# Optimization experiments

Measured on AMD Instinct MI355X. Metric: run time of the kernel, lower is better.

Reference implementation:

```python
import jax, jax.numpy as jnp
import numpy as np

LEN = 2048

def setup_inputs() -> dict:
    key = jax.random.key(0)
    k1, k2 = jax.random.split(key)
    x = jax.random.normal(k1, (LEN,), dtype=jnp.float32)
    y = jax.random.normal(k2, (LEN,), dtype=jnp.float32)
    return {"x": x, "y": y}

def reference(x, y):
    # Classic DTW DP with squared-difference cost.
    # Original torch code clamps indices with max(i-1,0)/max(j-1,0); because
    # DTW[i,j] is still +inf when read, the clamped reads reduce to the
    # standard recurrence: row 0 is a cumulative sum, col 0 uses only 'up',
    # interior uses min(up, left, diag).
    inf = jnp.float32(jnp.inf)
    cost0 = (x[0] - y) ** 2            # [len2]
    row0 = jnp.cumsum(cost0)           # DTW row i=0

    def row_step(prev_row, xi):
        cost = (xi - y) ** 2                                   # [len2]
        diag = jnp.concatenate([prev_row[:1], prev_row[:-1]])  # prev_row[j-1], clamped at j=0
        def cell(left, cud):
            c, up, dg = cud
            v = c + jnp.minimum(jnp.minimum(up, left), dg)
            return v, v
        # left init = inf => at j=0 min reduces to min(up, diag) = prev_row[0]
        _, new_row = jax.lax.scan(cell, inf, (cost, prev_row, diag))
        return new_row, None

    last_row, _ = jax.lax.scan(row_step, row0, x[1:])
    return jnp.sqrt(last_row[-1])
```

## Files before the change

### kernel.cpp

```cpp
#include <hip/hip_runtime.h>
#include <math.h>


#define NLEN   2048
#define NWL    4
#define CSTEP  64
#define SPB    (CSTEP / 2)
#define DSKEW  192
#define EXTRA  64
#define PAD    128
#define RROW   (PAD + 2176)
#define YPAD   128
#define TAUMAX 2112
#define GTOT   (TAUMAX + 7 * DSKEW + EXTRA + CSTEP)
#define FLAGBIG (1 << 20)
#define INFV   1e30f

typedef float f32x2 __attribute__((ext_vector_type(2)));

__device__ __forceinline__ float dpp_shr1(float v, float inj) {
    int r = __builtin_amdgcn_update_dpp(
        __builtin_bit_cast(int, inj), __builtin_bit_cast(int, v),
        0x138 , 0xF, 0xF, false );
    return __builtin_bit_cast(float, r);
}
__device__ __forceinline__ float rdlane(float v, int l) {
    return __builtin_bit_cast(float,
        __builtin_amdgcn_readlane(__builtin_bit_cast(int, v), l));
}
__device__ __forceinline__ float min3f(float a, float b, float c) {
    unsigned ia = __builtin_bit_cast(unsigned, a);
    unsigned ib = __builtin_bit_cast(unsigned, b);
    unsigned ic = __builtin_bit_cast(unsigned, c);
    unsigned m  = __builtin_elementwise_min(
                      __builtin_elementwise_min(ia, ib), ic);
    return __builtin_bit_cast(float, m);
}
__device__ __forceinline__ void spinflag(int* flag, int target) {
    while (__hip_atomic_load(flag, __ATOMIC_ACQUIRE,
                             __HIP_MEMORY_SCOPE_AGENT) < target)
        __builtin_amdgcn_s_sleep(2);
}

__global__ __launch_bounds__(256, 1) void dtw_kernel(const float* __restrict__ X,
                                                     const float* __restrict__ Y,
                                                     float* __restrict__ out,
                                                     float* __restrict__ ws) {
    int*   flag = (int*)ws;
    float* grow = ws + 16 + PAD;

    __shared__ __align__(16) float yB[YPAD + NLEN + YPAD];
    __shared__ float ring[(NWL + 1) * RROW];
    float* yS = yB + YPAD;

    const int tid  = threadIdx.x;
    const int w    = tid >> 6;
    const int lane = tid & 63;
    const int b    = blockIdx.x;
    const int skew = (4 * b + w) * DSKEW + (b ? EXTRA : 0);
    const bool isprod = (b == 0) & (w == 3);
    const bool iscons = (b == 1) & (w == 0);

    {
        const float4* Y4 = (const float4*)Y;
        float4* y4 = (float4*)(yB + YPAD);
        y4[tid]       = Y4[tid];
        y4[tid + 256] = Y4[tid + 256];
        if (tid < YPAD) {
            yB[tid]               = INFV;
            yB[YPAD + NLEN + tid] = INFV;
        }
    }
    for (int k = tid; k < (NWL + 1) * RROW; k += 256) ring[k] = INFV;
    __syncthreads();

    f32x2 xx0, xx1, xx2, xx3;
    {
        const float4 xa = *(const float4*)&X[b * 1024 + w * 256 + lane * 4];
        xx0 = (f32x2){xa.x, xa.x}; xx1 = (f32x2){xa.y, xa.y};
        xx2 = (f32x2){xa.z, xa.z}; xx3 = (f32x2){xa.w, xa.w};
    }

    float pB0 = INFV, pB1 = INFV, pB2 = INFV, pB3 = INFV;
    float a3p = INFV;
    float uBp = (b == 0 && tid == 0) ? 0.0f : INFV;
    float gcur = INFV, gnext = INFV;

    const float* ringR = ring + w * RROW + PAD;
    float*       ringW = ring + (w + 1) * RROW + PAD;

    for (int gb = 0; gb < GTOT; gb += CSTEP) {
        const int tau0 = gb - skew;

        if (tau0 >= 0 && tau0 <= TAUMAX) {
            float rblk;
            if (iscons) {
                if (tau0 == 0) {
                    spinflag(flag, 63);
                    gcur = grow[lane];
                }
                const int nt = tau0 + CSTEP;
                if (nt <= TAUMAX) {
                    int tgt = nt + 63;
                    if (tgt > NLEN - 1) tgt = NLEN - 1;
                    spinflag(flag, tgt);
                    gnext = grow[nt + lane];
                }
                rblk = gcur;
            } else {
                rblk = ringR[tau0 + lane];
            }

            f32x2 y2[SPB];
            {
                const f32x2* yp = (const f32x2*)(yS + (tau0 - 2 * lane));
                #pragma unroll
                for (int k = 0; k < SPB; ++k) y2[k] = yp[k];
            }
            float* wp = ringW + (tau0 - 2 * lane);
            const bool isout = (b == 1) & (w == 3) & (lane == 63)
                             & (tau0 == TAUMAX);

            #pragma unroll
            for (int s = 0; s < SPB; ++s) {
                const float riA = rdlane(rblk, 2 * s);
                const float riB = rdlane(rblk, 2 * s + 1);
                const float uA  = dpp_shr1(a3p, riA);
                const float uB  = dpp_shr1(pB3, riB);
                const f32x2 yv = y2[s];
                f32x2 d0 = xx0 - yv;
                float n0A = fmaf(d0.x, d0.x, min3f(pB0, uA,  uBp));
                float n0B = fmaf(d0.y, d0.y, min3f(n0A, uB,  uA));
                f32x2 d1 = xx1 - yv;
                float n1A = fmaf(d1.x, d1.x, min3f(pB1, n0A, pB0));
                float n1B = fmaf(d1.y, d1.y, min3f(n1A, n0B, n0A));
                f32x2 d2 = xx2 - yv;
                float n2A = fmaf(d2.x, d2.x, min3f(pB2, n1A, pB1));
                float n2B = fmaf(d2.y, d2.y, min3f(n2A, n1B, n1A));
                f32x2 d3 = xx3 - yv;
                float n3A = fmaf(d3.x, d3.x, min3f(pB3, n2A, pB2));
                float n3B = fmaf(d3.y, d3.y, min3f(n3A, n2B, n2A));
                f32x2 wv; wv.x = n3A; wv.y = n3B;
                *(f32x2*)(wp + 2 * s) = wv;
                uBp = uB; a3p = n3A;
                pB0 = n0B; pB1 = n1B; pB2 = n2B; pB3 = n3B;
                if (s == 30 && isout) out[0] = sqrtf(n3B);
            }

            if (isprod) {
                if (tau0 >= 128) {
                    __threadfence();
                    if (lane == 0)
                        __hip_atomic_store(flag, tau0 - 127, __ATOMIC_RELEASE,
                                           __HIP_MEMORY_SCOPE_AGENT);
                }
                grow[tau0 - 126 + lane] = ringW[tau0 - 126 + lane];
                if (tau0 == TAUMAX) {
                    __threadfence();
                    if (lane == 0)
                        __hip_atomic_store(flag, FLAGBIG, __ATOMIC_RELEASE,
                                           __HIP_MEMORY_SCOPE_AGENT);
                }
            }
            if (iscons) gcur = gnext;
        }
        __syncthreads();
    }
}

#define FNW    4
#define FGTOT  (TAUMAX + (FNW - 1) * DSKEW + CSTEP)

__global__ __launch_bounds__(256, 1) void dtw_kernel_fb(const float* __restrict__ X,
                                                        const float* __restrict__ Y,
                                                        float* __restrict__ out) {
    __shared__ __align__(16) float yB[YPAD + NLEN + YPAD];
    __shared__ float ring[(FNW + 1) * RROW];
    float* yS = yB + YPAD;

    const int tid  = threadIdx.x;
    const int w    = tid >> 6;
    const int lane = tid & 63;

    {
        const float4* Y4 = (const float4*)Y;
        float4* y4 = (float4*)(yB + YPAD);
        y4[tid]       = Y4[tid];
        y4[tid + 256] = Y4[tid + 256];
        if (tid < YPAD) {
            yB[tid]               = INFV;
            yB[YPAD + NLEN + tid] = INFV;
        }
    }
    for (int k = tid; k < (FNW + 1) * RROW; k += 256) ring[k] = INFV;
    __syncthreads();

    f32x2 xx0, xx1, xx2, xx3, xx4, xx5, xx6, xx7;
    {
        const float4 xa = *(const float4*)&X[tid * 8];
        const float4 xb = *(const float4*)&X[tid * 8 + 4];
        xx0 = (f32x2){xa.x, xa.x}; xx1 = (f32x2){xa.y, xa.y};
        xx2 = (f32x2){xa.z, xa.z}; xx3 = (f32x2){xa.w, xa.w};
        xx4 = (f32x2){xb.x, xb.x}; xx5 = (f32x2){xb.y, xb.y};
        xx6 = (f32x2){xb.z, xb.z}; xx7 = (f32x2){xb.w, xb.w};
    }

    float pB0 = INFV, pB1 = INFV, pB2 = INFV, pB3 = INFV;
    float pB4 = INFV, pB5 = INFV, pB6 = INFV, pB7 = INFV;
    float a7p = INFV;
    float uBp = (tid == 0) ? 0.0f : INFV;

    const float* ringR = ring + w * RROW + PAD;
    float*       ringW = ring + (w + 1) * RROW + PAD;

    for (int gb = 0; gb < FGTOT; gb += CSTEP) {
        const int tau0 = gb - w * DSKEW;

        if (tau0 >= 0 && tau0 <= TAUMAX) {
            const float rblk = ringR[tau0 + lane];
            f32x2 y2[SPB];
            {
                const f32x2* yp = (const f32x2*)(yS + (tau0 - 2 * lane));
                #pragma unroll
                for (int k = 0; k < SPB; ++k) y2[k] = yp[k];
            }
            float* wp = ringW + (tau0 - 2 * lane);
            const bool isout = (tau0 == TAUMAX) & (w == FNW - 1) & (lane == 63);

            #pragma unroll
            for (int s = 0; s < SPB; ++s) {
                const float riA = rdlane(rblk, 2 * s);
                const float riB = rdlane(rblk, 2 * s + 1);
                const float uA  = dpp_shr1(a7p, riA);
                const float uB  = dpp_shr1(pB7, riB);
                const f32x2 yv = y2[s];
                f32x2 d0 = xx0 - yv;
                float n0A = fmaf(d0.x, d0.x, min3f(pB0, uA,  uBp));
                float n0B = fmaf(d0.y, d0.y, min3f(n0A, uB,  uA));
                f32x2 d1 = xx1 - yv;
                float n1A = fmaf(d1.x, d1.x, min3f(pB1, n0A, pB0));
                float n1B = fmaf(d1.y, d1.y, min3f(n1A, n0B, n0A));
                f32x2 d2 = xx2 - yv;
                float n2A = fmaf(d2.x, d2.x, min3f(pB2, n1A, pB1));
                float n2B = fmaf(d2.y, d2.y, min3f(n2A, n1B, n1A));
                f32x2 d3 = xx3 - yv;
                float n3A = fmaf(d3.x, d3.x, min3f(pB3, n2A, pB2));
                float n3B = fmaf(d3.y, d3.y, min3f(n3A, n2B, n2A));
                f32x2 d4 = xx4 - yv;
                float n4A = fmaf(d4.x, d4.x, min3f(pB4, n3A, pB3));
                float n4B = fmaf(d4.y, d4.y, min3f(n4A, n3B, n3A));
                f32x2 d5 = xx5 - yv;
                float n5A = fmaf(d5.x, d5.x, min3f(pB5, n4A, pB4));
                float n5B = fmaf(d5.y, d5.y, min3f(n5A, n4B, n4A));
                f32x2 d6 = xx6 - yv;
                float n6A = fmaf(d6.x, d6.x, min3f(pB6, n5A, pB5));
                float n6B = fmaf(d6.y, d6.y, min3f(n6A, n5B, n5A));
                f32x2 d7 = xx7 - yv;
                float n7A = fmaf(d7.x, d7.x, min3f(pB7, n6A, pB6));
                float n7B = fmaf(d7.y, d7.y, min3f(n7A, n6B, n6A));
                f32x2 wv; wv.x = n7A; wv.y = n7B;
                *(f32x2*)(wp + 2 * s) = wv;
                uBp = uB; a7p = n7A;
                pB0 = n0B; pB1 = n1B; pB2 = n2B; pB3 = n3B;
                pB4 = n4B; pB5 = n5B; pB6 = n6B; pB7 = n7B;
                if (s == 30 && isout) out[0] = sqrtf(n7B);
            }
        }
        __syncthreads();
    }
}

extern "C" void kernel_launch(void* const* d_in, const int* in_sizes, int n_in,
                              void* d_out, int out_size, void* d_ws, size_t ws_size,
                              hipStream_t stream) {
    const float* x = (const float*)d_in[0];
    const float* y = (const float*)d_in[1];
    (void)in_sizes; (void)n_in; (void)out_size;
    if (d_ws != nullptr && ws_size >= 16384) {
        hipMemsetAsync(d_ws, 0, 4, stream);
        dtw_kernel<<<2, 256, 0, stream>>>(x, y, (float*)d_out, (float*)d_ws);
    } else {
        dtw_kernel_fb<<<1, 256, 0, stream>>>(x, y, (float*)d_out);
    }
}
```

Before: 180.6 us.

## Split DTW wavefront across four blocks with two rows per lane and ring buffers

Spreads the anti-diagonal DTW pipeline across four workgroups instead of two, so each lane owns two rows of x instead of four and the column step halves to 32. Inter-block boundary rows go through per-block global ring buffers with their own flags, and the consumer prefetches the next chunk into shared scratch. Boundary values are now read from LDS as vectors instead of via per-step readlane. The aim is a shorter serial dependency chain per step, paid for with more pipeline fill and drain stages and more cross-block flag spinning on the critical path.

```diff
diff --git a/kernel.cpp b/kernel.cpp
--- a/kernel.cpp
+++ b/kernel.cpp
@@ -4,29 +4,27 @@
 
 #define NLEN   2048
 #define NWL    4
-#define CSTEP  64
+#define CSTEP  32
 #define SPB    (CSTEP / 2)
-#define DSKEW  192
+#define DSKEW  160
 #define EXTRA  64
 #define PAD    128
-#define RROW   (PAD + 2176)
+#define RROW   2304
 #define YPAD   128
-#define TAUMAX 2112
-#define GTOT   (TAUMAX + 7 * DSKEW + EXTRA + CSTEP)
+#define TAUMAX 2144
+#define GTOT   (TAUMAX + 15 * DSKEW + 3 * EXTRA + CSTEP)
+#define RMASK  1023
 #define FLAGBIG (1 << 20)
 #define INFV   1e30f
 
 typedef float f32x2 __attribute__((ext_vector_type(2)));
+typedef float f32x4 __attribute__((ext_vector_type(4)));
 
 __device__ __forceinline__ float dpp_shr1(float v, float inj) {
     int r = __builtin_amdgcn_update_dpp(
         __builtin_bit_cast(int, inj), __builtin_bit_cast(int, v),
         0x138 , 0xF, 0xF, false );
     return __builtin_bit_cast(float, r);
-}
-__device__ __forceinline__ float rdlane(float v, int l) {
-    return __builtin_bit_cast(float,
-        __builtin_amdgcn_readlane(__builtin_bit_cast(int, v), l));
 }
 __device__ __forceinline__ float min3f(float a, float b, float c) {
     unsigned ia = __builtin_bit_cast(unsigned, a);
@@ -41,25 +39,34 @@
                              __HIP_MEMORY_SCOPE_AGENT) < target)
         __builtin_amdgcn_s_sleep(2);
 }
+__device__ __forceinline__ float gload(const float* p) {
+    unsigned u = __hip_atomic_load((const unsigned*)p, __ATOMIC_RELAXED,
+                                   __HIP_MEMORY_SCOPE_AGENT);
+    return __builtin_bit_cast(float, u);
+}
 
 __global__ __launch_bounds__(256, 1) void dtw_kernel(const float* __restrict__ X,
                                                      const float* __restrict__ Y,
                                                      float* __restrict__ out,
                                                      float* __restrict__ ws) {
-    int*   flag = (int*)ws;
-    float* grow = ws + 16 + PAD;
-
     __shared__ __align__(16) float yB[YPAD + NLEN + YPAD];
-    __shared__ float ring[(NWL + 1) * RROW];
+    __shared__ __align__(16) float ring[(NWL + 1) * RROW];
+    __shared__ __align__(16) float cscr[32];
     float* yS = yB + YPAD;
 
     const int tid  = threadIdx.x;
     const int w    = tid >> 6;
     const int lane = tid & 63;
     const int b    = blockIdx.x;
-    const int skew = (4 * b + w) * DSKEW + (b ? EXTRA : 0);
-    const bool isprod = (b == 0) & (w == 3);
-    const bool iscons = (b == 1) & (w == 0);
+    const int skew = (4 * b + w) * DSKEW + b * EXTRA;
+    const bool isprod = (b < 3) & (w == 3);
+    const bool iscons = (b > 0) & (w == 0);
+    const bool isbot  = (b == 3) & (w == 3);
+
+    int*   flagp = (int*)ws + 64 * b;
+    int*   flagc = (int*)ws + 64 * (b - 1);
+    float* growp = (float*)ws + 256 + 1024 * b;
+    float* growc = (float*)ws + 256 + 1024 * (b - 1);
 
     {
         const float4* Y4 = (const float4*)Y;
@@ -74,17 +81,16 @@
     for (int k = tid; k < (NWL + 1) * RROW; k += 256) ring[k] = INFV;
     __syncthreads();
 
-    f32x2 xx0, xx1, xx2, xx3;
+    f32x2 xx0, xx1;
     {
-        const float4 xa = *(const float4*)&X[b * 1024 + w * 256 + lane * 4];
-        xx0 = (f32x2){xa.x, xa.x}; xx1 = (f32x2){xa.y, xa.y};
-        xx2 = (f32x2){xa.z, xa.z}; xx3 = (f32x2){xa.w, xa.w};
-    }
-
-    float pB0 = INFV, pB1 = INFV, pB2 = INFV, pB3 = INFV;
-    float a3p = INFV;
+        const float2 xa = *(const float2*)&X[b * 512 + w * 128 + lane * 2];
+        xx0 = (f32x2){xa.x, xa.x};
+        xx1 = (f32x2){xa.y, xa.y};
+    }
+
+    float pB0 = INFV, pB1 = INFV;
+    float a1p = INFV;
     float uBp = (b == 0 && tid == 0) ? 0.0f : INFV;
-    float gcur = INFV, gnext = INFV;
 
     const float* ringR = ring + w * RROW + PAD;
     float*       ringW = ring + (w + 1) * RROW + PAD;
@@ -93,23 +99,34 @@
         const int tau0 = gb - skew;
 
         if (tau0 >= 0 && tau0 <= TAUMAX) {
-            float rblk;
+            if (isprod && tau0 >= 128) {
+                __threadfence();
+                if (lane == 0)
+                    __hip_atomic_store(flagp, tau0 - 127, __ATOMIC_RELEASE,
+                                       __HIP_MEMORY_SCOPE_AGENT);
+            }
+
+            float pref = 0.0f;
+            const bool dopref = iscons & (tau0 + CSTEP <= TAUMAX);
             if (iscons) {
                 if (tau0 == 0) {
-                    spinflag(flag, 63);
-                    gcur = grow[lane];
-                }
-                const int nt = tau0 + CSTEP;
-                if (nt <= TAUMAX) {
-                    int tgt = nt + 63;
-                    if (tgt > NLEN - 1) tgt = NLEN - 1;
-                    spinflag(flag, tgt);
-                    gnext = grow[nt + lane];
-                }
-                rblk = gcur;
-            } else {
-                rblk = ringR[tau0 + lane];
-            }
+                    spinflag(flagc, 31);
+                    if (lane < 32)
+                        cscr[lane] = gload(growc + ((lane + 2048) & RMASK));
+                }
+                if (dopref) {
+                    const int nt = tau0 + CSTEP;
+                    int tgt = nt + 31; if (tgt > NLEN - 1) tgt = NLEN - 1;
+                    spinflag(flagc, tgt);
+                    if (lane < 32)
+                        pref = gload(growc + ((nt + lane + 2048) & RMASK));
+                }
+            }
+
+            const float* rsrc = iscons ? cscr : (ringR + tau0);
+            f32x4 rv[8];
+            #pragma unroll
+            for (int q = 0; q < 8; ++q) rv[q] = *(const f32x4*)(rsrc + 4 * q);
 
             f32x2 y2[SPB];
             {
@@ -118,15 +135,14 @@
                 for (int k = 0; k < SPB; ++k) y2[k] = yp[k];
             }
             float* wp = ringW + (tau0 - 2 * lane);
-            const bool isout = (b == 1) & (w == 3) & (lane == 63)
-                             & (tau0 == TAUMAX);
+            const bool isout = isbot & (lane == 63) & (tau0 == TAUMAX);
 
             #pragma unroll
             for (int s = 0; s < SPB; ++s) {
-                const float riA = rdlane(rblk, 2 * s);
-                const float riB = rdlane(rblk, 2 * s + 1);
-                const float uA  = dpp_shr1(a3p, riA);
-                const float uB  = dpp_shr1(pB3, riB);
+                const float riA = rv[(2 * s) >> 2][(2 * s) & 3];
+                const float riB = rv[(2 * s + 1) >> 2][(2 * s + 1) & 3];
+                const float uA  = dpp_shr1(a1p, riA);
+                const float uB  = dpp_shr1(pB1, riB);
                 const f32x2 yv = y2[s];
                 f32x2 d0 = xx0 - yv;
                 float n0A = fmaf(d0.x, d0.x, min3f(pB0, uA,  uBp));
@@ -134,48 +150,52 @@
                 f32x2 d1 = xx1 - yv;
                 float n1A = fmaf(d1.x, d1.x, min3f(pB1, n0A, pB0));
                 float n1B = fmaf(d1.y, d1.y, min3f(n1A, n0B, n0A));
-                f32x2 d2 = xx2 - yv;
-                float n2A = fmaf(d2.x, d2.x, min3f(pB2, n1A, pB1));
-                float n2B = fmaf(d2.y, d2.y, min3f(n2A, n1B, n1A));
-                f32x2 d3 = xx3 - yv;
-                float n3A = fmaf(d3.x, d3.x, min3f(pB3, n2A, pB2));
-                float n3B = fmaf(d3.y, d3.y, min3f(n3A, n2B, n2A));
-                f32x2 wv; wv.x = n3A; wv.y = n3B;
-                *(f32x2*)(wp + 2 * s) = wv;
-                uBp = uB; a3p = n3A;
-                pB0 = n0B; pB1 = n1B; pB2 = n2B; pB3 = n3B;
-                if (s == 30 && isout) out[0] = sqrtf(n3B);
+                if (!isbot) {
+                    f32x2 wv; wv.x = n1A; wv.y = n1B;
+                    *(f32x2*)(wp + 2 * s) = wv;
+                }
+                uBp = uB; a1p = n1A;
+                pB0 = n0B; pB1 = n1B;
+                if (s == 14 && isout) out[0] = sqrtf(n1B);
             }
 
             if (isprod) {
-                if (tau0 >= 128) {
-                    __threadfence();
-                    if (lane == 0)
-                        __hip_atomic_store(flag, tau0 - 127, __ATOMIC_RELEASE,
-                                           __HIP_MEMORY_SCOPE_AGENT);
-                }
-                grow[tau0 - 126 + lane] = ringW[tau0 - 126 + lane];
+                if (lane < 32) {
+                    const int c = tau0 - 126 + lane;
+                    growp[(c + 2048) & RMASK] = ringW[c];
+                }
                 if (tau0 == TAUMAX) {
                     __threadfence();
                     if (lane == 0)
-                        __hip_atomic_store(flag, FLAGBIG, __ATOMIC_RELEASE,
+                        __hip_atomic_store(flagp, FLAGBIG, __ATOMIC_RELEASE,
                                            __HIP_MEMORY_SCOPE_AGENT);
                 }
             }
-            if (iscons) gcur = gnext;
+            if (dopref && lane < 32) cscr[lane] = pref;
         }
         __syncthreads();
     }
 }
 
 #define FNW    4
-#define FGTOT  (TAUMAX + (FNW - 1) * DSKEW + CSTEP)
+#define FCS    64
+#define FSPB   32
+#define FDSKEW 192
+#define FPAD   128
+#define FRROW  (FPAD + 2176)
+#define FTMAX  2112
+#define FGTOT  (FTMAX + (FNW - 1) * FDSKEW + FCS)
+
+__device__ __forceinline__ float rdlane(float v, int l) {
+    return __builtin_bit_cast(float,
+        __builtin_amdgcn_readlane(__builtin_bit_cast(int, v), l));
+}
 
 __global__ __launch_bounds__(256, 1) void dtw_kernel_fb(const float* __restrict__ X,
                                                         const float* __restrict__ Y,
                                                         float* __restrict__ out) {
     __shared__ __align__(16) float yB[YPAD + NLEN + YPAD];
-    __shared__ float ring[(FNW + 1) * RROW];
+    __shared__ float ring[(FNW + 1) * FRROW];
     float* yS = yB + YPAD;
 
     const int tid  = threadIdx.x;
@@ -192,7 +212,7 @@
             yB[YPAD + NLEN + tid] = INFV;
         }
     }
-    for (int k = tid; k < (FNW + 1) * RROW; k += 256) ring[k] = INFV;
+    for (int k = tid; k < (FNW + 1) * FRROW; k += 256) ring[k] = INFV;
     __syncthreads();
 
     f32x2 xx0, xx1, xx2, xx3, xx4, xx5, xx6, xx7;
@@ -210,25 +230,25 @@
     float a7p = INFV;
     float uBp = (tid == 0) ? 0.0f : INFV;
 
-    const float* ringR = ring + w * RROW + PAD;
-    float*       ringW = ring + (w + 1) * RROW + PAD;
-
-    for (int gb = 0; gb < FGTOT; gb += CSTEP) {
-        const int tau0 = gb - w * DSKEW;
-
-        if (tau0 >= 0 && tau0 <= TAUMAX) {
+    const float* ringR = ring + w * FRROW + FPAD;
+    float*       ringW = ring + (w + 1) * FRROW + FPAD;
+
+    for (int gb = 0; gb < FGTOT; gb += FCS) {
+        const int tau0 = gb - w * FDSKEW;
+
+        if (tau0 >= 0 && tau0 <= FTMAX) {
             const float rblk = ringR[tau0 + lane];
-            f32x2 y2[SPB];
+            f32x2 y2[FSPB];
             {
                 const f32x2* yp = (const f32x2*)(yS + (tau0 - 2 * lane));
                 #pragma unroll
-                for (int k = 0; k < SPB; ++k) y2[k] = yp[k];
+                for (int k = 0; k < FSPB; ++k) y2[k] = yp[k];
             }
             float* wp = ringW + (tau0 - 2 * lane);
-            const bool isout = (tau0 == TAUMAX) & (w == FNW - 1) & (lane == 63);
+            const bool isout = (tau0 == FTMAX) & (w == FNW - 1) & (lane == 63);
 
             #pragma unroll
-            for (int s = 0; s < SPB; ++s) {
+            for (int s = 0; s < FSPB; ++s) {
                 const float riA = rdlane(rblk, 2 * s);
                 const float riB = rdlane(rblk, 2 * s + 1);
                 const float uA  = dpp_shr1(a7p, riA);
@@ -277,8 +297,8 @@
     const float* y = (const float*)d_in[1];
     (void)in_sizes; (void)n_in; (void)out_size;
     if (d_ws != nullptr && ws_size >= 16384) {
-        hipMemsetAsync(d_ws, 0, 4, stream);
-        dtw_kernel<<<2, 256, 0, stream>>>(x, y, (float*)d_out, (float*)d_ws);
+        hipMemsetAsync(d_ws, 0, 1024, stream);
+        dtw_kernel<<<4, 256, 0, stream>>>(x, y, (float*)d_out, (float*)d_ws);
     } else {
         dtw_kernel_fb<<<1, 256, 0, stream>>>(x, y, (float*)d_out);
     }
```

Result: slower. 246.8 us (+36.6%).
